# Kernel optimization log

Measured on AMD Instinct MI355X. Metric: run time of the kernel, lower is better.

## Reference

```python
import jax, jax.numpy as jnp
import numpy as np

B, NF, H = 1024, 64, 512


def setup_inputs() -> dict:
    key = jax.random.key(0)
    ks = jax.random.split(key, 12)
    sc_in2 = 1.0 / np.sqrt(2 * H)
    sc_in1 = 1.0 / np.sqrt(H)
    inp = {
        "field_vectors": jax.random.normal(ks[0], (B, NF, H), dtype=jnp.float32),
        # and_fusion: Linear(2H->H), ReLU, Linear(H->H)
        "and_W1": jax.random.uniform(ks[1], (2 * H, H), jnp.float32, -sc_in2, sc_in2),
        "and_b1": jax.random.uniform(ks[2], (H,), jnp.float32, -sc_in2, sc_in2),
        "and_W2": jax.random.uniform(ks[3], (H, H), jnp.float32, -sc_in1, sc_in1),
        "and_b2": jax.random.uniform(ks[4], (H,), jnp.float32, -sc_in1, sc_in1),
        # or_fusion: Linear(2H->H), ReLU, Linear(H->H)
        "or_W1": jax.random.uniform(ks[5], (2 * H, H), jnp.float32, -sc_in2, sc_in2),
        "or_b1": jax.random.uniform(ks[6], (H,), jnp.float32, -sc_in2, sc_in2),
        "or_W2": jax.random.uniform(ks[7], (H, H), jnp.float32, -sc_in1, sc_in1),
        "or_b2": jax.random.uniform(ks[8], (H,), jnp.float32, -sc_in1, sc_in1),
        # not_transform: Linear(H->H), Tanh
        "not_W": jax.random.uniform(ks[9], (H, H), jnp.float32, -sc_in1, sc_in1),
        "not_b": jax.random.uniform(ks[10], (H,), jnp.float32, -sc_in1, sc_in1),
        # Disjoint index structure so the torch skip-set logic is a no-op:
        # 'and' pairs use fields 0..31, 'or' pairs use 32..47, leftovers 48..63.
        "not_idx": 48 + jnp.arange(8, dtype=jnp.int32),
        "and_pairs": jnp.arange(32, dtype=jnp.int32).reshape(16, 2),
        "or_pairs": (32 + jnp.arange(16, dtype=jnp.int32)).reshape(8, 2),
        "leftover_idx": 48 + jnp.arange(16, dtype=jnp.int32),
    }
    return inp


def _mlp2(x, W1, b1, W2, b2):
    # Linear -> ReLU -> Linear
    return jax.nn.relu(x @ W1 + b1) @ W2 + b2


def reference(field_vectors, and_W1, and_b1, and_W2, and_b2,
              or_W1, or_b1, or_W2, or_b2, not_W, not_b,
              not_idx, and_pairs, or_pairs, leftover_idx):
    # In-place 'not' transform on selected fields (Tanh(Linear))
    fv = field_vectors.at[:, not_idx].set(
        jnp.tanh(field_vectors[:, not_idx] @ not_W + not_b))
    # Gather (i, j) pairs, concat along feature dim -> [B, P, 2H]
    cat_and = jnp.concatenate([fv[:, and_pairs[:, 0]], fv[:, and_pairs[:, 1]]], axis=-1)
    fused_and = _mlp2(cat_and, and_W1, and_b1, and_W2, and_b2)  # [B, 16, H]
    cat_or = jnp.concatenate([fv[:, or_pairs[:, 0]], fv[:, or_pairs[:, 1]]], axis=-1)
    fused_or = _mlp2(cat_or, or_W1, or_b1, or_W2, or_b2)  # [B, 8, H]
    # Stack order matches torch loop: and results, or results, untouched fields
    return jnp.concatenate([fused_and, fused_or, fv[:, leftover_idx]], axis=1)
```

## Files before the change

kernel.cpp:

```cpp
#include <hip/hip_runtime.h>
#include <hip/hip_bf16.h>
#include <math.h>

typedef __attribute__((ext_vector_type(8))) __bf16 bf16x8;
typedef __attribute__((ext_vector_type(4))) float f32x4;

__device__ __forceinline__ unsigned short f2bf(float f) {
    union { float f; unsigned u; } v; v.f = f;
    unsigned r = v.u + 0x7fffu + ((v.u >> 16) & 1u);
    return (unsigned short)(r >> 16);
}
__device__ __forceinline__ unsigned int pk(float a, float b) {
    union { float f; unsigned u; } x, y; x.f = a; y.f = b;
    unsigned ra = (x.u + 0x7fffu + ((x.u >> 16) & 1u)) >> 16;
    unsigned rb = (y.u + 0x7fffu + ((y.u >> 16) & 1u)) & 0xffff0000u;
    return ra | rb;
}

__device__ __forceinline__ void gl2lds16(const unsigned short* g, unsigned short* l) {
    __builtin_amdgcn_global_load_lds(
        (const __attribute__((address_space(1))) unsigned int*)(g),
        (__attribute__((address_space(3))) unsigned int*)(l), 16, 0, 0);
}

struct SetupArgs {
    const int *and_pairs, *or_pairs, *not_idx, *lidx;
    int* tbl;
    const float* W[5];
    unsigned short* WT[5];
    int K[5], N[5];
    int tstart[6];
};

__global__ __launch_bounds__(256) void setup_kernel(SetupArgs a) {
    __shared__ float tile[64][65];
    const int blk = blockIdx.x;
    const int tid = threadIdx.x;

    if (blk == 0) {
        if (tid < 64) {
            const int f = tid;
            int u = 0;
            for (int i = 0; i < 32; i++) u |= (a.and_pairs[i] == f);
            for (int i = 0; i < 16; i++) u |= (a.or_pairs[i] == f);
            int isnot = 0;
            for (int i = 0; i < 8; i++)  isnot |= (a.not_idx[i] == f);
            int ls = -1;
            for (int l = 0; l < 16; l++) if (a.lidx[l] == f) ls = l;
            if (isnot) ls = -1;
            a.tbl[f] = (u | isnot) | ((ls + 1) << 8);
        }
        return;
    }

    const int bx = blk - 1;
    int m = 0;
    while (bx >= a.tstart[m + 1]) m++;
    const float* src = a.W[m];
    unsigned short* dst = a.WT[m];
    const int K = a.K[m], N = a.N[m];
    const int t = bx - a.tstart[m];
    const int ntn = N >> 6;
    const int tk = t / ntn, tn = t % ntn;
    const int c = tid & 63, r0 = tid >> 6;
    #pragma unroll
    for (int r = r0; r < 64; r += 4)
        tile[r][c] = src[(size_t)(tk * 64 + r) * N + tn * 64 + c];
    __syncthreads();
    #pragma unroll
    for (int r = r0; r < 64; r += 4)
        dst[(size_t)(tn * 64 + r) * K + tk * 64 + c] = f2bf(tile[c][r]);
}

struct PrepArgs {
    const float* fv;
    unsigned short* fvb;
    const int* tbl;
    float* out;
};

__global__ __launch_bounds__(256) void prep_kernel(PrepArgs a) {
    const int t = blockIdx.x * 256 + threadIdx.x;
    const size_t e = (size_t)t * 8;
    const int c = (int)(e & 511);
    const int f = (int)((e >> 9) & 63);
    const int b = (int)(e >> 15);
    const float4 v0 = *(const float4*)(a.fv + e);
    const float4 v1 = *(const float4*)(a.fv + e + 4);
    const int tb = a.tbl[f];
    const int u  = tb & 0xff;
    const int ls = (tb >> 8) - 1;
    if (u) {
        uint4 o;
        o.x = pk(v0.x, v0.y); o.y = pk(v0.z, v0.w);
        o.z = pk(v1.x, v1.y); o.w = pk(v1.z, v1.w);
        ((uint4*)a.fvb)[t] = o;
    }
    if (ls >= 0) {
        float* d = a.out + ((size_t)b * 40 + 24 + ls) * 512 + c;
        *(float4*)(d)     = v0;
        *(float4*)(d + 4) = v1;
    }
}

template <int P, int K, int SRCM, int EPIM, int QBASE>
__device__ __forceinline__ void gemm_seg(
    const unsigned short* __restrict__ A,
    const int* __restrict__ idx,
    const unsigned short* __restrict__ WT,
    const float* __restrict__ bias,
    unsigned short* __restrict__ hid_out,
    float* __restrict__ out,
    const int* __restrict__ leftover,
    int local,
    unsigned short* As, unsigned short* Bs) {

    const int tid  = threadIdx.x;
    const int lane = tid & 63, w = tid >> 6;
    const int tm = (local >> 2) * 128, tn = (local & 3) * 128;

    const int lm  = lane >> 2;
    const int kin = (((lane & 3) ^ ((lane >> 2) & 3)) * 8);
    const unsigned short* ar0[2];
    const unsigned short* ar1[2];
    const unsigned short* wp[2];
    #pragma unroll
    for (int c = 0; c < 2; c++) {
        const int m = tm + w * 32 + c * 16 + lm;
        if constexpr (SRCM == 0) {
            const int b = m / P, p = m % P;
            ar0[c] = A + ((size_t)b * 64 + idx[2 * p]) * 512;
            ar1[c] = A + ((size_t)b * 64 + idx[2 * p + 1]) * 512;
        } else if constexpr (SRCM == 1) {
            const int b = m >> 3, i = m & 7;
            ar0[c] = A + ((size_t)b * 64 + idx[i]) * 512;
        } else {
            ar0[c] = A + (size_t)m * K;
        }
        const int n = tn + w * 32 + c * 16 + lm;
        wp[c] = WT + (size_t)n * K;
    }

    f32x4 acc[4][4];
    #pragma unroll
    for (int i = 0; i < 4; i++)
        #pragma unroll
        for (int j = 0; j < 4; j++)
            acc[i][j] = f32x4{0.f, 0.f, 0.f, 0.f};

    const int wm = (w & 1) * 64, wn = (w >> 1) * 64;
    const int xsel = ((lane >> 4) ^ (lane & 3)) * 8;

    auto stage = [&](int buf, int k0) {
        #pragma unroll
        for (int c = 0; c < 2; c++) {
            const unsigned short* asrc;
            if constexpr (SRCM == 0)
                asrc = (k0 >= 512 ? ar1[c] + (k0 - 512) : ar0[c] + k0) + kin;
            else
                asrc = ar0[c] + k0 + kin;
            gl2lds16(asrc, &As[buf * 4096 + w * 1024 + c * 512]);
            gl2lds16(wp[c] + k0 + kin, &Bs[buf * 4096 + w * 1024 + c * 512]);
        }
    };

    constexpr int NT = K / 32;
    stage(0, 0);
    __syncthreads();

    for (int t = 0; t < NT; t++) {
        const int cur = t & 1;
        if (t + 1 < NT) stage(cur ^ 1, (t + 1) * 32);
        const unsigned short* Ab = &As[cur * 4096];
        const unsigned short* Bb = &Bs[cur * 4096];
        bf16x8 af[4], bfr[4];
        #pragma unroll
        for (int mi = 0; mi < 4; mi++)
            af[mi] = *(const bf16x8*)&Ab[(wm + mi * 16 + (lane & 15)) * 32 + xsel];
        #pragma unroll
        for (int ni = 0; ni < 4; ni++)
            bfr[ni] = *(const bf16x8*)&Bb[(wn + ni * 16 + (lane & 15)) * 32 + xsel];
        #pragma unroll
        for (int mi = 0; mi < 4; mi++)
            #pragma unroll
            for (int ni = 0; ni < 4; ni++)
                acc[mi][ni] = __builtin_amdgcn_mfma_f32_16x16x32_bf16(
                    af[mi], bfr[ni], acc[mi][ni], 0, 0, 0);
        __syncthreads();
    }

    const int col0 = tn + wn + (lane & 15);
    const int row0 = tm + wm + (lane >> 4) * 4;

    int qmap[8];
    if constexpr (EPIM == 2) {
        #pragma unroll
        for (int i = 0; i < 8; i++) {
            const int f = idx[i];
            int q = 24;
            for (int l = 0; l < 16; l++)
                if (leftover[l] == f) q = 24 + l;
            qmap[i] = q;
        }
    }

    #pragma unroll
    for (int ni = 0; ni < 4; ni++) {
        const int n  = col0 + ni * 16;
        const float bv = bias[n];
        #pragma unroll
        for (int mi = 0; mi < 4; mi++) {
            const int rbase = row0 + mi * 16;
            #pragma unroll
            for (int j = 0; j < 4; j++) {
                const int m = rbase + j;
                float v = acc[mi][ni][j] + bv;
                if constexpr (EPIM == 0) {
                    v = v > 0.f ? v : 0.f;
                    hid_out[(size_t)m * 512 + n] = f2bf(v);
                } else if constexpr (EPIM == 1) {
                    const int b = m / P, p = m % P;
                    out[((size_t)b * 40 + QBASE + p) * 512 + n] = v;
                } else {
                    const int b = m >> 3, i = m & 7;
                    out[((size_t)b * 40 + qmap[i]) * 512 + n] = tanhf(v);
                }
            }
        }
    }
}

struct L1Args {
    const unsigned short *fvb, *and_W1T, *or_W1T, *not_WT;
    const int *and_pairs, *or_pairs, *not_idx, *leftover;
    const float *and_b1, *or_b1, *not_b;
    unsigned short *and_hid, *or_hid;
    float* out;
};

__global__ __launch_bounds__(256, 4) void l1_phase(L1Args a) {
    __shared__ __align__(16) unsigned short As[2 * 128 * 32];
    __shared__ __align__(16) unsigned short Bs[2 * 128 * 32];
    const int blk = blockIdx.x;
    if (blk < 512)
        gemm_seg<16, 1024, 0, 0, 0>(a.fvb, a.and_pairs, a.and_W1T, a.and_b1,
                                    a.and_hid, nullptr, nullptr, blk, As, Bs);
    else if (blk < 768)
        gemm_seg<8, 1024, 0, 0, 0>(a.fvb, a.or_pairs, a.or_W1T, a.or_b1,
                                   a.or_hid, nullptr, nullptr, blk - 512, As, Bs);
    else
        gemm_seg<8, 512, 1, 2, 24>(a.fvb, a.not_idx, a.not_WT, a.not_b,
                                   nullptr, a.out, a.leftover, blk - 768, As, Bs);
}

struct L2Args {
    const unsigned short *and_hid, *or_hid, *and_W2T, *or_W2T;
    const float *and_b2, *or_b2;
    float* out;
};

__global__ __launch_bounds__(256, 4) void l2_phase(L2Args a) {
    __shared__ __align__(16) unsigned short As[2 * 128 * 32];
    __shared__ __align__(16) unsigned short Bs[2 * 128 * 32];
    const int blk = blockIdx.x;
    if (blk < 512)
        gemm_seg<16, 512, 2, 1, 0>(a.and_hid, nullptr, a.and_W2T, a.and_b2,
                                   nullptr, a.out, nullptr, blk, As, Bs);
    else
        gemm_seg<8, 512, 2, 1, 16>(a.or_hid, nullptr, a.or_W2T, a.or_b2,
                                   nullptr, a.out, nullptr, blk - 512, As, Bs);
}

extern "C" void kernel_launch(void* const* d_in, const int* in_sizes, int n_in,
                              void* d_out, int out_size, void* d_ws, size_t ws_size,
                              hipStream_t stream) {
    const float* fv       = (const float*)d_in[0];
    const float* and_W1   = (const float*)d_in[1];
    const float* and_b1   = (const float*)d_in[2];
    const float* and_W2   = (const float*)d_in[3];
    const float* and_b2   = (const float*)d_in[4];
    const float* or_W1    = (const float*)d_in[5];
    const float* or_b1    = (const float*)d_in[6];
    const float* or_W2    = (const float*)d_in[7];
    const float* or_b2    = (const float*)d_in[8];
    const float* not_W    = (const float*)d_in[9];
    const float* not_b    = (const float*)d_in[10];
    const int* not_idx    = (const int*)d_in[11];
    const int* and_pairs  = (const int*)d_in[12];
    const int* or_pairs   = (const int*)d_in[13];
    const int* leftover   = (const int*)d_in[14];
    float* out = (float*)d_out;
    char* ws = (char*)d_ws;

    unsigned short* fvb     = (unsigned short*)(ws);
    unsigned short* and_W1T = (unsigned short*)(ws + 67108864);
    unsigned short* or_W1T  = (unsigned short*)(ws + 68157440);
    unsigned short* and_W2T = (unsigned short*)(ws + 69206016);
    unsigned short* or_W2T  = (unsigned short*)(ws + 69730304);
    unsigned short* not_WT  = (unsigned short*)(ws + 70254592);
    unsigned short* and_hid = (unsigned short*)(ws + 70778880);
    unsigned short* or_hid  = (unsigned short*)(ws + 87556096);
    int*            tbl     = (int*)(ws + 95944704);

    SetupArgs sa;
    sa.and_pairs = and_pairs; sa.or_pairs = or_pairs;
    sa.not_idx = not_idx; sa.lidx = leftover; sa.tbl = tbl;
    sa.W[0] = and_W1; sa.WT[0] = and_W1T; sa.K[0] = 1024; sa.N[0] = 512;
    sa.W[1] = or_W1;  sa.WT[1] = or_W1T;  sa.K[1] = 1024; sa.N[1] = 512;
    sa.W[2] = and_W2; sa.WT[2] = and_W2T; sa.K[2] = 512;  sa.N[2] = 512;
    sa.W[3] = or_W2;  sa.WT[3] = or_W2T;  sa.K[3] = 512;  sa.N[3] = 512;
    sa.W[4] = not_W;  sa.WT[4] = not_WT;  sa.K[4] = 512;  sa.N[4] = 512;
    sa.tstart[0] = 0;   sa.tstart[1] = 128; sa.tstart[2] = 256;
    sa.tstart[3] = 320; sa.tstart[4] = 384; sa.tstart[5] = 448;
    setup_kernel<<<dim3(449), dim3(256), 0, stream>>>(sa);

    PrepArgs pa;
    pa.fv = fv; pa.fvb = fvb; pa.tbl = tbl; pa.out = out;
    prep_kernel<<<dim3(16384), dim3(256), 0, stream>>>(pa);

    L1Args g1;
    g1.fvb = fvb; g1.and_W1T = and_W1T; g1.or_W1T = or_W1T; g1.not_WT = not_WT;
    g1.and_pairs = and_pairs; g1.or_pairs = or_pairs; g1.not_idx = not_idx;
    g1.leftover = leftover;
    g1.and_b1 = and_b1; g1.or_b1 = or_b1; g1.not_b = not_b;
    g1.and_hid = and_hid; g1.or_hid = or_hid; g1.out = out;
    l1_phase<<<dim3(1024), dim3(256), 0, stream>>>(g1);

    L2Args g2;
    g2.and_hid = and_hid; g2.or_hid = or_hid;
    g2.and_W2T = and_W2T; g2.or_W2T = or_W2T;
    g2.and_b2 = and_b2; g2.or_b2 = or_b2; g2.out = out;
    l2_phase<<<dim3(768), dim3(256), 0, stream>>>(g2);
}
```

Baseline: 340.9 us.

## Fuse both MLP layers into one kernel keeping hidden activations in LDS

Merges the two GEMM phases into a single kernel. Each block computes a 64-row by 512-column tile of the first layer, applies bias and ReLU, writes the bf16 hidden tile into a swizzled LDS buffer, and then runs the second layer from LDS. B operands are now loaded straight from global memory into registers with double buffering, and only A is staged through LDS. This removes the global hidden-activation round trip and a kernel launch, at the cost of 64 KB+ LDS per block, 2 blocks/CU occupancy, more accumulator registers, and weights re-read from global/L2 by every block.

Result: slower. 359.4 us (+5.4%).

```diff
diff --git a/kernel.cpp b/kernel.cpp
--- a/kernel.cpp
+++ b/kernel.cpp
@@ -103,97 +103,95 @@
     }
 }
 
-template <int P, int K, int SRCM, int EPIM, int QBASE>
-__device__ __forceinline__ void gemm_seg(
+#define LOADB(DST, WTP, KD, K0)                                              \
+    _Pragma("unroll") for (int ni = 0; ni < 8; ni++)                         \
+        DST[ni] = *(const bf16x8*)((WTP) +                                   \
+            (size_t)(wn + ni * 16 + ln15) * (KD) + (K0) + kq * 8);
+
+#define MMAC(BF, AF)                                                         \
+    _Pragma("unroll") for (int mi = 0; mi < 4; mi++)                         \
+    _Pragma("unroll") for (int ni = 0; ni < 8; ni++)                         \
+        acc[mi][ni] = __builtin_amdgcn_mfma_f32_16x16x32_bf16(               \
+            AF[mi], BF[ni], acc[mi][ni], 0, 0, 0);
+
+template <int P, int K1, int SRCM, int PATH, int QBASE>
+__device__ __forceinline__ void fused_seg(
     const unsigned short* __restrict__ A,
     const int* __restrict__ idx,
-    const unsigned short* __restrict__ WT,
-    const float* __restrict__ bias,
-    unsigned short* __restrict__ hid_out,
+    const unsigned short* __restrict__ W1T,
+    const float* __restrict__ b1,
+    const unsigned short* __restrict__ W2T,
+    const float* __restrict__ b2,
     float* __restrict__ out,
     const int* __restrict__ leftover,
     int local,
-    unsigned short* As, unsigned short* Bs) {
+    unsigned short* As, unsigned short* hid) {
 
     const int tid  = threadIdx.x;
     const int lane = tid & 63, w = tid >> 6;
-    const int tm = (local >> 2) * 128, tn = (local & 3) * 128;
-
-    const int lm  = lane >> 2;
-    const int kin = (((lane & 3) ^ ((lane >> 2) & 3)) * 8);
-    const unsigned short* ar0[2];
-    const unsigned short* ar1[2];
-    const unsigned short* wp[2];
-    #pragma unroll
-    for (int c = 0; c < 2; c++) {
-        const int m = tm + w * 32 + c * 16 + lm;
+    const int ln15 = lane & 15;
+    const int kq   = lane >> 4;
+    const int wn   = w * 128;
+    const int m0   = local * 64;
+
+    const int skin = ((lane & 3) ^ ((lane >> 2) & 3)) * 8;
+    const unsigned short *ar0, *ar1;
+    {
+        const int m = m0 + w * 16 + (lane >> 2);
         if constexpr (SRCM == 0) {
             const int b = m / P, p = m % P;
-            ar0[c] = A + ((size_t)b * 64 + idx[2 * p]) * 512;
-            ar1[c] = A + ((size_t)b * 64 + idx[2 * p + 1]) * 512;
-        } else if constexpr (SRCM == 1) {
+            ar0 = A + ((size_t)b * 64 + idx[2 * p]) * 512;
+            ar1 = A + ((size_t)b * 64 + idx[2 * p + 1]) * 512;
+        } else {
             const int b = m >> 3, i = m & 7;
-            ar0[c] = A + ((size_t)b * 64 + idx[i]) * 512;
-        } else {
-            ar0[c] = A + (size_t)m * K;
-        }
-        const int n = tn + w * 32 + c * 16 + lm;
-        wp[c] = WT + (size_t)n * K;
-    }
-
-    f32x4 acc[4][4];
-    #pragma unroll
-    for (int i = 0; i < 4; i++)
-        #pragma unroll
-        for (int j = 0; j < 4; j++)
-            acc[i][j] = f32x4{0.f, 0.f, 0.f, 0.f};
-
-    const int wm = (w & 1) * 64, wn = (w >> 1) * 64;
-    const int xsel = ((lane >> 4) ^ (lane & 3)) * 8;
-
-    auto stage = [&](int buf, int k0) {
-        #pragma unroll
-        for (int c = 0; c < 2; c++) {
-            const unsigned short* asrc;
-            if constexpr (SRCM == 0)
-                asrc = (k0 >= 512 ? ar1[c] + (k0 - 512) : ar0[c] + k0) + kin;
-            else
-                asrc = ar0[c] + k0 + kin;
-            gl2lds16(asrc, &As[buf * 4096 + w * 1024 + c * 512]);
-            gl2lds16(wp[c] + k0 + kin, &Bs[buf * 4096 + w * 1024 + c * 512]);
-        }
+            ar0 = A + ((size_t)b * 64 + idx[i]) * 512;
+            ar1 = ar0;
+        }
+    }
+    auto stageA = [&](int buf, int t) {
+        const int k0 = t * 32;
+        const unsigned short* src;
+        if constexpr (SRCM == 0)
+            src = (k0 >= 512 ? ar1 + (k0 - 512) : ar0 + k0) + skin;
+        else
+            src = ar0 + k0 + skin;
+        gl2lds16(src, &As[buf * 2048 + w * 512]);
     };
-
-    constexpr int NT = K / 32;
-    stage(0, 0);
+    const int xsel = (kq ^ (lane & 3)) * 8;
+
+    f32x4 acc[4][8];
+    #pragma unroll
+    for (int mi = 0; mi < 4; mi++)
+        #pragma unroll
+        for (int ni = 0; ni < 8; ni++)
+            acc[mi][ni] = f32x4{0.f, 0.f, 0.f, 0.f};
+
+    bf16x8 bA[8], bB[8];
+
+    constexpr int NT1 = K1 / 32;
+    stageA(0, 0);
+    LOADB(bA, W1T, K1, 0);
     __syncthreads();
-
-    for (int t = 0; t < NT; t++) {
-        const int cur = t & 1;
-        if (t + 1 < NT) stage(cur ^ 1, (t + 1) * 32);
-        const unsigned short* Ab = &As[cur * 4096];
-        const unsigned short* Bb = &Bs[cur * 4096];
-        bf16x8 af[4], bfr[4];
+    for (int t = 0; t < NT1; t += 2) {
+        stageA(1, t + 1);
+        bf16x8 af[4];
         #pragma unroll
         for (int mi = 0; mi < 4; mi++)
-            af[mi] = *(const bf16x8*)&Ab[(wm + mi * 16 + (lane & 15)) * 32 + xsel];
-        #pragma unroll
-        for (int ni = 0; ni < 4; ni++)
-            bfr[ni] = *(const bf16x8*)&Bb[(wn + ni * 16 + (lane & 15)) * 32 + xsel];
+            af[mi] = *(const bf16x8*)&As[(mi * 16 + ln15) * 32 + xsel];
+        LOADB(bB, W1T, K1, (t + 1) * 32);
+        MMAC(bA, af);
+        __syncthreads();
+        if (t + 2 < NT1) stageA(0, t + 2);
         #pragma unroll
         for (int mi = 0; mi < 4; mi++)
-            #pragma unroll
-            for (int ni = 0; ni < 4; ni++)
-                acc[mi][ni] = __builtin_amdgcn_mfma_f32_16x16x32_bf16(
-                    af[mi], bfr[ni], acc[mi][ni], 0, 0, 0);
+            af[mi] = *(const bf16x8*)&As[2048 + (mi * 16 + ln15) * 32 + xsel];
+        if (t + 2 < NT1) { LOADB(bA, W1T, K1, (t + 2) * 32); }
+        MMAC(bB, af);
         __syncthreads();
     }
 
-    const int col0 = tn + wn + (lane & 15);
-    const int row0 = tm + wm + (lane >> 4) * 4;
-
-    int qmap[8];
-    if constexpr (EPIM == 2) {
+    if constexpr (PATH == 2) {
+        int qmap[8];
         #pragma unroll
         for (int i = 0; i < 8; i++) {
             const int f = idx[i];
@@ -202,73 +200,111 @@
                 if (leftover[l] == f) q = 24 + l;
             qmap[i] = q;
         }
-    }
-
-    #pragma unroll
-    for (int ni = 0; ni < 4; ni++) {
-        const int n  = col0 + ni * 16;
-        const float bv = bias[n];
-        #pragma unroll
-        for (int mi = 0; mi < 4; mi++) {
-            const int rbase = row0 + mi * 16;
+        #pragma unroll
+        for (int ni = 0; ni < 8; ni++) {
+            const int n = wn + ni * 16 + ln15;
+            const float bv = b1[n];
+            #pragma unroll
+            for (int mi = 0; mi < 4; mi++)
+                #pragma unroll
+                for (int j = 0; j < 4; j++) {
+                    const int r = mi * 16 + kq * 4 + j;
+                    const int m = m0 + r;
+                    const int b = m >> 3, i = m & 7;
+                    out[((size_t)b * 40 + qmap[i]) * 512 + n] =
+                        tanhf(acc[mi][ni][j] + bv);
+                }
+        }
+        return;
+    }
+
+    #pragma unroll
+    for (int ni = 0; ni < 8; ni++) {
+        const int n  = wn + ni * 16 + ln15;
+        const float bv = b1[n];
+        const int c8 = n >> 3;
+        const int cl = (n & 7) * 2;
+        #pragma unroll
+        for (int mi = 0; mi < 4; mi++)
             #pragma unroll
             for (int j = 0; j < 4; j++) {
-                const int m = rbase + j;
+                const int r = mi * 16 + kq * 4 + j;
                 float v = acc[mi][ni][j] + bv;
-                if constexpr (EPIM == 0) {
-                    v = v > 0.f ? v : 0.f;
-                    hid_out[(size_t)m * 512 + n] = f2bf(v);
-                } else if constexpr (EPIM == 1) {
-                    const int b = m / P, p = m % P;
-                    out[((size_t)b * 40 + QBASE + p) * 512 + n] = v;
-                } else {
-                    const int b = m >> 3, i = m & 7;
-                    out[((size_t)b * 40 + qmap[i]) * 512 + n] = tanhf(v);
-                }
+                v = v > 0.f ? v : 0.f;
+                *(unsigned short*)((char*)hid + r * 1024 +
+                                   ((c8 ^ (r & 7)) * 16) + cl) = f2bf(v);
             }
-        }
-    }
-}
-
-struct L1Args {
-    const unsigned short *fvb, *and_W1T, *or_W1T, *not_WT;
+    }
+    #pragma unroll
+    for (int mi = 0; mi < 4; mi++)
+        #pragma unroll
+        for (int ni = 0; ni < 8; ni++)
+            acc[mi][ni] = f32x4{0.f, 0.f, 0.f, 0.f};
+    LOADB(bA, W2T, 512, 0);
+    __syncthreads();
+
+    for (int t2 = 0; t2 < 16; t2 += 2) {
+        bf16x8 af[4];
+        #pragma unroll
+        for (int mi = 0; mi < 4; mi++) {
+            const int r = mi * 16 + ln15;
+            const int c8 = t2 * 4 + kq;
+            af[mi] = *(const bf16x8*)((char*)hid + r * 1024 +
+                                      ((c8 ^ (r & 7)) * 16));
+        }
+        LOADB(bB, W2T, 512, (t2 + 1) * 32);
+        MMAC(bA, af);
+        #pragma unroll
+        for (int mi = 0; mi < 4; mi++) {
+            const int r = mi * 16 + ln15;
+            const int c8 = (t2 + 1) * 4 + kq;
+            af[mi] = *(const bf16x8*)((char*)hid + r * 1024 +
+                                      ((c8 ^ (r & 7)) * 16));
+        }
+        if (t2 + 2 < 16) { LOADB(bA, W2T, 512, (t2 + 2) * 32); }
+        MMAC(bB, af);
+    }
+
+    #pragma unroll
+    for (int ni = 0; ni < 8; ni++) {
+        const int n  = wn + ni * 16 + ln15;
+        const float bv = b2[n];
+        #pragma unroll
+        for (int mi = 0; mi < 4; mi++)
+            #pragma unroll
+            for (int j = 0; j < 4; j++) {
+                const int r = mi * 16 + kq * 4 + j;
+                const int m = m0 + r;
+                const int b = m / P, p = m % P;
+                out[((size_t)b * 40 + QBASE + p) * 512 + n] =
+                    acc[mi][ni][j] + bv;
+            }
+    }
+}
+
+struct FArgs {
+    const unsigned short *fvb, *and_W1T, *and_W2T, *or_W1T, *or_W2T, *not_WT;
     const int *and_pairs, *or_pairs, *not_idx, *leftover;
-    const float *and_b1, *or_b1, *not_b;
-    unsigned short *and_hid, *or_hid;
+    const float *and_b1, *and_b2, *or_b1, *or_b2, *not_b;
     float* out;
 };
 
-__global__ __launch_bounds__(256, 4) void l1_phase(L1Args a) {
-    __shared__ __align__(16) unsigned short As[2 * 128 * 32];
-    __shared__ __align__(16) unsigned short Bs[2 * 128 * 32];
+__global__ __launch_bounds__(256, 2) void fused_phase(FArgs a) {
+    __shared__ __align__(16) unsigned short As[2 * 64 * 32];
+    __shared__ __align__(16) unsigned short hid[64 * 512];
     const int blk = blockIdx.x;
-    if (blk < 512)
-        gemm_seg<16, 1024, 0, 0, 0>(a.fvb, a.and_pairs, a.and_W1T, a.and_b1,
-                                    a.and_hid, nullptr, nullptr, blk, As, Bs);
-    else if (blk < 768)
-        gemm_seg<8, 1024, 0, 0, 0>(a.fvb, a.or_pairs, a.or_W1T, a.or_b1,
-                                   a.or_hid, nullptr, nullptr, blk - 512, As, Bs);
+    if (blk < 256)
+        fused_seg<16, 1024, 0, 0, 0>(a.fvb, a.and_pairs, a.and_W1T, a.and_b1,
+                                     a.and_W2T, a.and_b2, a.out, nullptr,
+                                     blk, As, hid);
+    else if (blk < 384)
+        fused_seg<8, 1024, 0, 0, 16>(a.fvb, a.or_pairs, a.or_W1T, a.or_b1,
+                                     a.or_W2T, a.or_b2, a.out, nullptr,
+                                     blk - 256, As, hid);
     else
-        gemm_seg<8, 512, 1, 2, 24>(a.fvb, a.not_idx, a.not_WT, a.not_b,
-                                   nullptr, a.out, a.leftover, blk - 768, As, Bs);
-}
-
-struct L2Args {
-    const unsigned short *and_hid, *or_hid, *and_W2T, *or_W2T;
-    const float *and_b2, *or_b2;
-    float* out;
-};
-
-__global__ __launch_bounds__(256, 4) void l2_phase(L2Args a) {
-    __shared__ __align__(16) unsigned short As[2 * 128 * 32];
-    __shared__ __align__(16) unsigned short Bs[2 * 128 * 32];
-    const int blk = blockIdx.x;
-    if (blk < 512)
-        gemm_seg<16, 512, 2, 1, 0>(a.and_hid, nullptr, a.and_W2T, a.and_b2,
-                                   nullptr, a.out, nullptr, blk, As, Bs);
-    else
-        gemm_seg<8, 512, 2, 1, 16>(a.or_hid, nullptr, a.or_W2T, a.or_b2,
-                                   nullptr, a.out, nullptr, blk - 512, As, Bs);
+        fused_seg<8, 512, 1, 2, 24>(a.fvb, a.not_idx, a.not_WT, a.not_b,
+                                    nullptr, nullptr, a.out, a.leftover,
+                                    blk - 384, As, hid);
 }
 
 extern "C" void kernel_launch(void* const* d_in, const int* in_sizes, int n_in,
@@ -298,9 +334,7 @@
     unsigned short* and_W2T = (unsigned short*)(ws + 69206016);
     unsigned short* or_W2T  = (unsigned short*)(ws + 69730304);
     unsigned short* not_WT  = (unsigned short*)(ws + 70254592);
-    unsigned short* and_hid = (unsigned short*)(ws + 70778880);
-    unsigned short* or_hid  = (unsigned short*)(ws + 87556096);
-    int*            tbl     = (int*)(ws + 95944704);
+    int*            tbl     = (int*)(ws + 70778880);
 
     SetupArgs sa;
     sa.and_pairs = and_pairs; sa.or_pairs = or_pairs;
@@ -318,17 +352,14 @@
     pa.fv = fv; pa.fvb = fvb; pa.tbl = tbl; pa.out = out;
     prep_kernel<<<dim3(16384), dim3(256), 0, stream>>>(pa);
 
-    L1Args g1;
-    g1.fvb = fvb; g1.and_W1T = and_W1T; g1.or_W1T = or_W1T; g1.not_WT = not_WT;
-    g1.and_pairs = and_pairs; g1.or_pairs = or_pairs; g1.not_idx = not_idx;
-    g1.leftover = leftover;
-    g1.and_b1 = and_b1; g1.or_b1 = or_b1; g1.not_b = not_b;
-    g1.and_hid = and_hid; g1.or_hid = or_hid; g1.out = out;
-    l1_phase<<<dim3(1024), dim3(256), 0, stream>>>(g1);
-
-    L2Args g2;
-    g2.and_hid = and_hid; g2.or_hid = or_hid;
-    g2.and_W2T = and_W2T; g2.or_W2T = or_W2T;
-    g2.and_b2 = and_b2; g2.or_b2 = or_b2; g2.out = out;
-    l2_phase<<<dim3(768), dim3(256), 0, stream>>>(g2);
-}
+    FArgs fa;
+    fa.fvb = fvb;
+    fa.and_W1T = and_W1T; fa.and_W2T = and_W2T;
+    fa.or_W1T = or_W1T;   fa.or_W2T = or_W2T;   fa.not_WT = not_WT;
+    fa.and_pairs = and_pairs; fa.or_pairs = or_pairs; fa.not_idx = not_idx;
+    fa.leftover = leftover;
+    fa.and_b1 = and_b1; fa.and_b2 = and_b2;
+    fa.or_b1 = or_b1;   fa.or_b2 = or_b2;   fa.not_b = not_b;
+    fa.out = out;
+    fused_phase<<<dim3(512), dim3(256), 0, stream>>>(fa);
+}
```
